# Kernel tuning notes

Hardware: AMD Instinct MI355X
Metric: run time of the kernel (lower is better)

## Reference

```python
import jax, jax.numpy as jnp
import numpy as np

# Config constants (mirror MoEConfig)
NUM_EXPERTS = 8
TOP_K = 2
CAPACITY_FACTOR = 1.25
TEMPERATURE = 1.0
LB_LOSS_WEIGHT = 0.01


def setup_inputs() -> dict:
    key = jax.random.key(0)
    k1, k2 = jax.random.split(key)
    B, S, H = 8, 4096, 1024
    hidden_states = jax.random.normal(k1, (B, S, H), dtype=jnp.float32)
    # nn.Linear weight, init std=0.02, no bias
    router_w = jax.random.normal(k2, (NUM_EXPERTS, H), dtype=jnp.float32) * 0.02
    return {"hidden_states": hidden_states, "router_w": router_w}


def _token_choice_routing(hidden_states, router_w):
    B, S, H = hidden_states.shape
    E = router_w.shape[0]
    N = B * S

    # Router (eval mode: no noise since noise_epsilon=0)
    router_logits = jnp.einsum('bsh,eh->bse', hidden_states, router_w) / TEMPERATURE
    router_probs = jax.nn.softmax(router_logits, axis=-1)

    # Top-k expert selection per token, renormalize weights
    expert_weights, expert_indices = jax.lax.top_k(router_probs, TOP_K)  # [B,S,K]
    expert_weights = expert_weights / expert_weights.sum(axis=-1, keepdims=True)

    # Scatter into dispatch mask [B,S,E] (top-k indices are unique per token)
    one_hot = jax.nn.one_hot(expert_indices, E, dtype=expert_weights.dtype)  # [B,S,K,E]
    dispatch_mask = jnp.einsum('bske,bsk->bse', one_hot, expert_weights)

    tokens_per_expert = dispatch_mask.sum(axis=(0, 1))  # [E]

    # Auxiliary load-balance loss
    expert_fraction = tokens_per_expert / N
    mean_prob = router_probs.mean(axis=(0, 1))
    load_balancing_loss = N * jnp.sum(expert_fraction * mean_prob) * LB_LOSS_WEIGHT

    # Capacity constraint: keep only top-`capacity` weights per expert over all tokens
    capacity = int(CAPACITY_FACTOR * S * B / E)
    flat = dispatch_mask.reshape(N, E).T  # [E, N]
    vals, idx = jax.lax.top_k(flat, capacity)  # [E, capacity]
    new_flat = jnp.zeros_like(flat).at[jnp.arange(E)[:, None], idx].set(vals)
    constrained = new_flat.T.reshape(B, S, E)
    # torch code only rewrites experts that exceed capacity
    over = tokens_per_expert > capacity  # [E]
    dispatch_mask = jnp.where(over, constrained, dispatch_mask)

    return dispatch_mask, load_balancing_loss, router_probs


def reference(hidden_states, router_w):
    dispatch_mask, lb_loss, router_probs = _token_choice_routing(hidden_states, router_w)
    # combine_weights == dispatch_mask in the original module
    return dispatch_mask, lb_loss, router_probs
```

## Files before the change

kernel.cpp:

```cpp
#include <hip/hip_runtime.h>

#define H 1024
#define E 8
#define BLK 256
#define CAP 5120
#define FBLK 1024

__global__ __launch_bounds__(BLK, 4) void router_kernel(
    const float* __restrict__ hs,
    const float* __restrict__ rw,
    float* __restrict__ dispatch,
    float* __restrict__ probs_out,
    float* __restrict__ partial)
{
    __shared__ float w_lds[E * H];

    const int tid = threadIdx.x;
    for (int i = tid; i < E * H / 4; i += BLK)
        ((float4*)w_lds)[i] = ((const float4*)rw)[i];
    __syncthreads();

    const int wave = tid >> 6;
    const int lane = tid & 63;
    const int t    = lane >> 4;
    const int f    = lane & 15;
    const int wid  = blockIdx.x * (BLK / 64) + wave;
    const size_t tok0 = (size_t)wid * 8 + t * 2;

    float acc0[E], acc1[E];
#pragma unroll
    for (int e = 0; e < E; ++e) { acc0[e] = 0.f; acc1[e] = 0.f; }

    const float* h0 = hs + tok0 * H + 4 * f;

    float4 a0 = *(const float4*)(h0);
    float4 a1 = *(const float4*)(h0 + H);
#pragma unroll 2
    for (int c = 0; c < 16; ++c) {
        float4 n0 = a0, n1 = a1;
        if (c < 15) {
            n0 = *(const float4*)(h0 + (c + 1) * 64);
            n1 = *(const float4*)(h0 + H + (c + 1) * 64);
        }
        const float* wb = w_lds + c * 64 + 4 * f;
#pragma unroll
        for (int eg = 0; eg < 2; ++eg) {
            float4 wv[4];
#pragma unroll
            for (int q = 0; q < 4; ++q)
                wv[q] = *(const float4*)(wb + (eg * 4 + q) * H);
#pragma unroll
            for (int q = 0; q < 4; ++q) {
                const int e = eg * 4 + q;
                acc0[e] = fmaf(a0.x, wv[q].x, acc0[e]);
                acc0[e] = fmaf(a0.y, wv[q].y, acc0[e]);
                acc0[e] = fmaf(a0.z, wv[q].z, acc0[e]);
                acc0[e] = fmaf(a0.w, wv[q].w, acc0[e]);
                acc1[e] = fmaf(a1.x, wv[q].x, acc1[e]);
                acc1[e] = fmaf(a1.y, wv[q].y, acc1[e]);
                acc1[e] = fmaf(a1.z, wv[q].z, acc1[e]);
                acc1[e] = fmaf(a1.w, wv[q].w, acc1[e]);
            }
        }
        a0 = n0; a1 = n1;
    }

#pragma unroll
    for (int e = 0; e < E; ++e) {
        float v0 = acc0[e], v1 = acc1[e];
        v0 += __shfl_xor(v0, 1); v1 += __shfl_xor(v1, 1);
        v0 += __shfl_xor(v0, 2); v1 += __shfl_xor(v1, 2);
        v0 += __shfl_xor(v0, 4); v1 += __shfl_xor(v1, 4);
        v0 += __shfl_xor(v0, 8); v1 += __shfl_xor(v1, 8);
        acc0[e] = v0; acc1[e] = v1;
    }

    const int se = f & 7;
    const int sk = f >> 3;
    float slotv = 0.f;

#pragma unroll
    for (int j = 0; j < 2; ++j) {
        const float* L = j ? acc1 : acc0;
        float mx = L[0];
#pragma unroll
        for (int e = 1; e < E; ++e) mx = fmaxf(mx, L[e]);
        float p[E], s = 0.f;
#pragma unroll
        for (int e = 0; e < E; ++e) { p[e] = expf(L[e] - mx); s += p[e]; }
        const float inv = 1.f / s;
#pragma unroll
        for (int e = 0; e < E; ++e) p[e] *= inv;

        int i1 = 0;
#pragma unroll
        for (int e = 1; e < E; ++e) if (p[e] > p[i1]) i1 = e;
        int i2 = -1;
#pragma unroll
        for (int e = 0; e < E; ++e) {
            if (e == i1) continue;
            if (i2 < 0 || p[e] > p[i2]) i2 = e;
        }
        const float s12 = p[i1] + p[i2];
        const float w1 = p[i1] / s12;
        const float w2 = p[i2] / s12;

        const size_t tok = tok0 + j;
        if (f < 8) {
            const float de = (f == i1) ? w1 : ((f == i2) ? w2 : 0.f);
            dispatch[tok * E + f] = de;
        } else {
            probs_out[tok * E + (f - 8)] = p[f - 8];
        }
        slotv += sk ? p[se] : ((se == i1) ? w1 : ((se == i2) ? w2 : 0.f));
    }

    __syncthreads();
    float* red = w_lds;
    red[wave * 64 + lane] = slotv;
    __syncthreads();
    if (tid < 16) {
        float s = 0.f;
#pragma unroll
        for (int k = 0; k < 16; ++k) s += red[k * 16 + tid];
        partial[(size_t)tid * gridDim.x + blockIdx.x] = s;
    }
}

__global__ __launch_bounds__(FBLK) void finalize_kernel(
    float* __restrict__ dispatch,
    const float* __restrict__ partial,
    int nb,
    float* __restrict__ lb_out,
    int N)
{
    const int e    = blockIdx.x;
    const int tid  = threadIdx.x;
    const int lane = tid & 63;
    const int wv   = tid >> 6;

    __shared__ float g[16];
    {
        float v = 0.f;
        for (int b = lane; b < nb; b += 64) v += partial[(size_t)wv * nb + b];
#pragma unroll
        for (int off = 32; off; off >>= 1) v += __shfl_xor(v, off);
        if (lane == 0) g[wv] = v;
    }
    __syncthreads();

    if (e == 0 && tid == 0) {
        float s = 0.f;
        for (int i = 0; i < E; ++i) s += g[i] * g[E + i];
        *lb_out = 0.01f * s / (float)N;
    }

    const float tpe = g[e];
    if (!(tpe > (float)CAP)) return;

    __shared__ unsigned hist[256];
    __shared__ unsigned sh_prefix;
    __shared__ int sh_k;

    unsigned prefix = 0;
    int k = CAP;

    for (int round = 0; round < 4; ++round) {
        const int shift = 24 - 8 * round;
        for (int i = tid; i < 256; i += FBLK) hist[i] = 0;
        __syncthreads();
        const unsigned mhi = (round == 0) ? 0u : (0xFFFFFFFFu << (shift + 8));
        for (int i = tid; i < N; i += FBLK) {
            const unsigned bits = __float_as_uint(dispatch[(size_t)i * E + e]);
            if ((bits & mhi) == (prefix & mhi))
                atomicAdd(&hist[(bits >> shift) & 255u], 1u);
        }
        __syncthreads();
        if (tid == 0) {
            int cum = 0;
            int d = 255;
            for (; d > 0; --d) {
                const int h = (int)hist[d];
                if (cum + h >= k) break;
                cum += h;
            }
            sh_prefix = prefix | ((unsigned)d << shift);
            sh_k = k - cum;
        }
        __syncthreads();
        prefix = sh_prefix;
        k = sh_k;
        __syncthreads();
    }

    const unsigned T = prefix;
    const unsigned r = (unsigned)k;

    __shared__ unsigned wave_cnt[FBLK / 64];
    __shared__ unsigned running;
    if (tid == 0) running = 0;
    __syncthreads();

    for (int base = 0; base < N; base += FBLK) {
        const int i = base + tid;
        const unsigned bits = __float_as_uint(dispatch[(size_t)i * E + e]);
        const bool eq = (bits == T);
        const unsigned long long bal = __ballot(eq);
        if (lane == 0) wave_cnt[wv] = (unsigned)__popcll(bal);
        __syncthreads();
        unsigned before = running;
        for (int w = 0; w < wv; ++w) before += wave_cnt[w];
        const unsigned rank = before + (unsigned)__popcll(bal & ((1ull << lane) - 1ull));
        const bool keep = (bits > T) || (eq && rank < r);
        if (!keep) dispatch[(size_t)i * E + e] = 0.f;
        __syncthreads();
        if (tid == 0) {
            unsigned tot = 0;
            for (int w = 0; w < FBLK / 64; ++w) tot += wave_cnt[w];
            running += tot;
        }
        __syncthreads();
    }
}

extern "C" void kernel_launch(void* const* d_in, const int* in_sizes, int n_in,
                              void* d_out, int out_size, void* d_ws, size_t ws_size,
                              hipStream_t stream)
{
    const float* hs = (const float*)d_in[0];
    const float* rw = (const float*)d_in[1];
    const int n_tokens = in_sizes[0] / H;

    float* dispatch = (float*)d_out;
    float* lb       = dispatch + (size_t)n_tokens * E;
    float* probs    = lb + 1;
    float* partial  = (float*)d_ws;

    const int nb = n_tokens / 32;
    router_kernel<<<nb, BLK, 0, stream>>>(hs, rw, dispatch, probs, partial);
    finalize_kernel<<<E, FBLK, 0, stream>>>(dispatch, partial, nb, lb, n_tokens);
}
```

Measured before the change: 214.5 us.

## Split router into logits and softmax kernels with deeper nontemporal prefetch

Splits the fused router kernel into a pure GEMV logits kernel and a separate per-token softmax/top-2 kernel that writes dispatch, probs and per-block partial sums. The logits kernel prefetches two chunks ahead with nontemporal loads and overlaps the first loads with the weight copy into shared memory. The goal is to keep the memory-bound GEMV streaming without the epilogue stalling it, and to use vectorized stores in the epilogue. In exchange it adds a round trip of the logits through workspace memory and an extra kernel launch.

```diff
diff --git a/kernel.cpp b/kernel.cpp
--- a/kernel.cpp
+++ b/kernel.cpp
@@ -6,19 +6,18 @@
 #define CAP 5120
 #define FBLK 1024
 
-__global__ __launch_bounds__(BLK, 4) void router_kernel(
+typedef float f32x4 __attribute__((ext_vector_type(4)));
+
+__global__ __launch_bounds__(BLK, 4) void logits_kernel(
     const float* __restrict__ hs,
     const float* __restrict__ rw,
-    float* __restrict__ dispatch,
-    float* __restrict__ probs_out,
-    float* __restrict__ partial)
+    float* __restrict__ logits)
 {
     __shared__ float w_lds[E * H];
 
     const int tid = threadIdx.x;
     for (int i = tid; i < E * H / 4; i += BLK)
-        ((float4*)w_lds)[i] = ((const float4*)rw)[i];
-    __syncthreads();
+        ((f32x4*)w_lds)[i] = ((const f32x4*)rw)[i];
 
     const int wave = tid >> 6;
     const int lane = tid & 63;
@@ -26,43 +25,48 @@
     const int f    = lane & 15;
     const int wid  = blockIdx.x * (BLK / 64) + wave;
     const size_t tok0 = (size_t)wid * 8 + t * 2;
+    const float* h0 = hs + tok0 * H + 4 * f;
+
+    f32x4 A0[2], A1[2];
+    A0[0] = __builtin_nontemporal_load((const f32x4*)(h0));
+    A1[0] = __builtin_nontemporal_load((const f32x4*)(h0 + H));
+    A0[1] = __builtin_nontemporal_load((const f32x4*)(h0 + 64));
+    A1[1] = __builtin_nontemporal_load((const f32x4*)(h0 + H + 64));
+
+    __syncthreads();
 
     float acc0[E], acc1[E];
 #pragma unroll
     for (int e = 0; e < E; ++e) { acc0[e] = 0.f; acc1[e] = 0.f; }
 
-    const float* h0 = hs + tok0 * H + 4 * f;
-
-    float4 a0 = *(const float4*)(h0);
-    float4 a1 = *(const float4*)(h0 + H);
 #pragma unroll 2
     for (int c = 0; c < 16; ++c) {
-        float4 n0 = a0, n1 = a1;
-        if (c < 15) {
-            n0 = *(const float4*)(h0 + (c + 1) * 64);
-            n1 = *(const float4*)(h0 + H + (c + 1) * 64);
+        const int cur = c & 1;
+        const f32x4 a0 = A0[cur], a1 = A1[cur];
+        if (c < 14) {
+            A0[cur] = __builtin_nontemporal_load((const f32x4*)(h0 + (c + 2) * 64));
+            A1[cur] = __builtin_nontemporal_load((const f32x4*)(h0 + H + (c + 2) * 64));
         }
         const float* wb = w_lds + c * 64 + 4 * f;
 #pragma unroll
         for (int eg = 0; eg < 2; ++eg) {
-            float4 wv[4];
+            f32x4 wv[4];
 #pragma unroll
             for (int q = 0; q < 4; ++q)
-                wv[q] = *(const float4*)(wb + (eg * 4 + q) * H);
+                wv[q] = *(const f32x4*)(wb + (eg * 4 + q) * H);
 #pragma unroll
             for (int q = 0; q < 4; ++q) {
                 const int e = eg * 4 + q;
-                acc0[e] = fmaf(a0.x, wv[q].x, acc0[e]);
-                acc0[e] = fmaf(a0.y, wv[q].y, acc0[e]);
-                acc0[e] = fmaf(a0.z, wv[q].z, acc0[e]);
-                acc0[e] = fmaf(a0.w, wv[q].w, acc0[e]);
-                acc1[e] = fmaf(a1.x, wv[q].x, acc1[e]);
-                acc1[e] = fmaf(a1.y, wv[q].y, acc1[e]);
-                acc1[e] = fmaf(a1.z, wv[q].z, acc1[e]);
-                acc1[e] = fmaf(a1.w, wv[q].w, acc1[e]);
+                acc0[e] = fmaf(a0[0], wv[q][0], acc0[e]);
+                acc0[e] = fmaf(a0[1], wv[q][1], acc0[e]);
+                acc0[e] = fmaf(a0[2], wv[q][2], acc0[e]);
+                acc0[e] = fmaf(a0[3], wv[q][3], acc0[e]);
+                acc1[e] = fmaf(a1[0], wv[q][0], acc1[e]);
+                acc1[e] = fmaf(a1[1], wv[q][1], acc1[e]);
+                acc1[e] = fmaf(a1[2], wv[q][2], acc1[e]);
+                acc1[e] = fmaf(a1[3], wv[q][3], acc1[e]);
             }
         }
-        a0 = n0; a1 = n1;
     }
 
 #pragma unroll
@@ -75,55 +79,78 @@
         acc0[e] = v0; acc1[e] = v1;
     }
 
-    const int se = f & 7;
-    const int sk = f >> 3;
-    float slotv = 0.f;
-
-#pragma unroll
-    for (int j = 0; j < 2; ++j) {
-        const float* L = j ? acc1 : acc0;
-        float mx = L[0];
-#pragma unroll
-        for (int e = 1; e < E; ++e) mx = fmaxf(mx, L[e]);
-        float p[E], s = 0.f;
-#pragma unroll
-        for (int e = 0; e < E; ++e) { p[e] = expf(L[e] - mx); s += p[e]; }
-        const float inv = 1.f / s;
-#pragma unroll
-        for (int e = 0; e < E; ++e) p[e] *= inv;
-
-        int i1 = 0;
-#pragma unroll
-        for (int e = 1; e < E; ++e) if (p[e] > p[i1]) i1 = e;
-        int i2 = -1;
-#pragma unroll
-        for (int e = 0; e < E; ++e) {
-            if (e == i1) continue;
-            if (i2 < 0 || p[e] > p[i2]) i2 = e;
-        }
-        const float s12 = p[i1] + p[i2];
-        const float w1 = p[i1] / s12;
-        const float w2 = p[i2] / s12;
-
-        const size_t tok = tok0 + j;
-        if (f < 8) {
-            const float de = (f == i1) ? w1 : ((f == i2) ? w2 : 0.f);
-            dispatch[tok * E + f] = de;
-        } else {
-            probs_out[tok * E + (f - 8)] = p[f - 8];
-        }
-        slotv += sk ? p[se] : ((se == i1) ? w1 : ((se == i2) ? w2 : 0.f));
-    }
-
-    __syncthreads();
-    float* red = w_lds;
-    red[wave * 64 + lane] = slotv;
+    const float outv = (f < 8) ? acc0[f] : acc1[f - 8];
+    logits[tok0 * 8 + f] = outv;
+}
+
+__global__ __launch_bounds__(256) void softmax_kernel(
+    const float* __restrict__ logits,
+    float* __restrict__ dispatch,
+    float* __restrict__ probs_out,
+    float* __restrict__ partial,
+    int nb2)
+{
+    __shared__ float red[4][16];
+    const int tid  = threadIdx.x;
+    const int lane = tid & 63;
+    const int wv   = tid >> 6;
+    const size_t tok = (size_t)blockIdx.x * 256 + tid;
+
+    const f32x4 l0 = *(const f32x4*)(logits + tok * 8);
+    const f32x4 l1 = *(const f32x4*)(logits + tok * 8 + 4);
+    float L[E] = {l0[0], l0[1], l0[2], l0[3], l1[0], l1[1], l1[2], l1[3]};
+
+    float mx = L[0];
+#pragma unroll
+    for (int e = 1; e < E; ++e) mx = fmaxf(mx, L[e]);
+    float p[E], s = 0.f;
+#pragma unroll
+    for (int e = 0; e < E; ++e) { p[e] = expf(L[e] - mx); s += p[e]; }
+    const float inv = 1.f / s;
+#pragma unroll
+    for (int e = 0; e < E; ++e) p[e] *= inv;
+
+    int i1 = 0;
+#pragma unroll
+    for (int e = 1; e < E; ++e) if (p[e] > p[i1]) i1 = e;
+    int i2 = -1;
+#pragma unroll
+    for (int e = 0; e < E; ++e) {
+        if (e == i1) continue;
+        if (i2 < 0 || p[e] > p[i2]) i2 = e;
+    }
+    const float s12 = p[i1] + p[i2];
+    const float w1 = p[i1] / s12;
+    const float w2 = p[i2] / s12;
+
+    float d[E];
+#pragma unroll
+    for (int e = 0; e < E; ++e) d[e] = (e == i1) ? w1 : ((e == i2) ? w2 : 0.f);
+
+    f32x4 v;
+    v[0] = d[0]; v[1] = d[1]; v[2] = d[2]; v[3] = d[3];
+    *(f32x4*)(dispatch + tok * 8) = v;
+    v[0] = d[4]; v[1] = d[5]; v[2] = d[6]; v[3] = d[7];
+    *(f32x4*)(dispatch + tok * 8 + 4) = v;
+    v[0] = p[0]; v[1] = p[1]; v[2] = p[2]; v[3] = p[3];
+    *(f32x4*)(probs_out + tok * 8) = v;
+    v[0] = p[4]; v[1] = p[5]; v[2] = p[6]; v[3] = p[7];
+    *(f32x4*)(probs_out + tok * 8 + 4) = v;
+
+#pragma unroll
+    for (int e = 0; e < E; ++e) {
+        float v1 = d[e], v2 = p[e];
+#pragma unroll
+        for (int off = 32; off; off >>= 1) {
+            v1 += __shfl_xor(v1, off);
+            v2 += __shfl_xor(v2, off);
+        }
+        if (lane == 0) { red[wv][e] = v1; red[wv][E + e] = v2; }
+    }
     __syncthreads();
     if (tid < 16) {
-        float s = 0.f;
-#pragma unroll
-        for (int k = 0; k < 16; ++k) s += red[k * 16 + tid];
-        partial[(size_t)tid * gridDim.x + blockIdx.x] = s;
+        const float s2 = red[0][tid] + red[1][tid] + red[2][tid] + red[3][tid];
+        partial[(size_t)tid * nb2 + blockIdx.x] = s2;
     }
 }
 
@@ -234,9 +261,14 @@
     float* dispatch = (float*)d_out;
     float* lb       = dispatch + (size_t)n_tokens * E;
     float* probs    = lb + 1;
-    float* partial  = (float*)d_ws;
-
-    const int nb = n_tokens / 32;
-    router_kernel<<<nb, BLK, 0, stream>>>(hs, rw, dispatch, probs, partial);
-    finalize_kernel<<<E, FBLK, 0, stream>>>(dispatch, partial, nb, lb, n_tokens);
-}
+
+    float* logits   = (float*)d_ws;
+    float* partial  = logits + (size_t)n_tokens * E;
+
+    const int nb1 = n_tokens / 32;
+    const int nb2 = n_tokens / 256;
+
+    logits_kernel<<<nb1, BLK, 0, stream>>>(hs, rw, logits);
+    softmax_kernel<<<nb2, 256, 0, stream>>>(logits, dispatch, probs, partial, nb2);
+    finalize_kernel<<<E, FBLK, 0, stream>>>(dispatch, partial, nb2, lb, n_tokens);
+}
```

New measurement: 207.5 us. 1.03x faster.
